# Kernel tuning notes

Hardware: AMD Instinct MI355X
Metric: run time of the kernel (lower is better)

Reference implementation:

```python
import jax, jax.numpy as jnp
import numpy as np

L, B, T, C, H = 8, 2, 1024, 1024, 16
DH = C // H          # 64, head dim (even, required for RoPE)
DFF = 4 * C          # 4096
THETA = 10000.0
EPS = 1e-5


def _ln(x, scale, bias):
    m = jnp.mean(x, axis=-1, keepdims=True)
    v = jnp.mean((x - m) ** 2, axis=-1, keepdims=True)
    return (x - m) * jax.lax.rsqrt(v + EPS) * scale + bias


def _rope_cos_sin():
    # matches precompute_freqs_cis: freqs_cis[t, j] = exp(i * t * theta^{-2j/dim})
    inv = 1.0 / (THETA ** (jnp.arange(0, DH, 2, dtype=jnp.float32) / DH))  # (DH/2,)
    ang = jnp.arange(T, dtype=jnp.float32)[:, None] * inv[None, :]         # (T, DH/2)
    return jnp.cos(ang), jnp.sin(ang)


def _apply_rope(x, cos, sin):
    # x: (B,H,T,DH); complex multiply on interleaved pairs == torch.view_as_complex path
    xr = x.reshape(B, H, T, DH // 2, 2)
    x0, x1 = xr[..., 0], xr[..., 1]
    o0 = x0 * cos - x1 * sin
    o1 = x0 * sin + x1 * cos
    return jnp.stack([o0, o1], axis=-1).reshape(B, H, T, DH)


def setup_inputs() -> dict:
    key = jax.random.key(0)
    ks = jax.random.split(key, 20)
    s = 0.02
    p = lambda k, shape: (jax.random.normal(k, shape, jnp.float32) * s)
    return {
        "x": jax.random.normal(ks[0], (B, T, C), jnp.float32),
        "Wq": p(ks[1], (L, C, C)), "bq": jnp.zeros((L, C), jnp.float32),
        "Wk": p(ks[2], (L, C, C)), "bk": jnp.zeros((L, C), jnp.float32),
        "Wv": p(ks[3], (L, C, C)), "bv": jnp.zeros((L, C), jnp.float32),
        "Wo": p(ks[4], (L, C, C)), "bo": jnp.zeros((L, C), jnp.float32),
        "ln1_s": jnp.ones((L, C), jnp.float32), "ln1_b": jnp.zeros((L, C), jnp.float32),
        "ln2_s": jnp.ones((L, C), jnp.float32), "ln2_b": jnp.zeros((L, C), jnp.float32),
        "W1": p(ks[5], (L, C, DFF)), "b1": jnp.zeros((L, DFF), jnp.float32),
        "W2": p(ks[6], (L, DFF, C)), "b2": jnp.zeros((L, C), jnp.float32),
        "lnf_s": jnp.ones((C,), jnp.float32), "lnf_b": jnp.zeros((C,), jnp.float32),
    }


def reference(x, Wq, bq, Wk, bk, Wv, bv, Wo, bo,
              ln1_s, ln1_b, ln2_s, ln2_b, W1, b1, W2, b2, lnf_s, lnf_b):
    cos, sin = _rope_cos_sin()
    causal = jnp.tril(jnp.ones((T, T), bool))
    inv_sqrt_dh = jnp.float32(1.0 / np.sqrt(DH))

    def layer(h, p):
        wq, bq_, wk, bk_, wv, bv_, wo, bo_, s1, c1, s2, c2, w1, d1, w2, d2 = p
        a = _ln(h, s1, c1)
        q = (a @ wq + bq_).reshape(B, T, H, DH).transpose(0, 2, 1, 3)  # (B,H,T,DH)
        k = (a @ wk + bk_).reshape(B, T, H, DH).transpose(0, 2, 1, 3)
        v = (a @ wv + bv_).reshape(B, T, H, DH).transpose(0, 2, 1, 3)
        q = _apply_rope(q, cos, sin)
        k = _apply_rope(k, cos, sin)
        att = jnp.einsum('bhqd,bhkd->bhqk', q, k) * inv_sqrt_dh
        att = jnp.where(causal, att, -jnp.inf)
        att = jax.nn.softmax(att, axis=-1)
        y = jnp.einsum('bhqk,bhkd->bhqd', att, v)
        y = y.transpose(0, 2, 1, 3).reshape(B, T, C)
        h = h + (y @ wo + bo_)
        m = _ln(h, s2, c2)
        h = h + (jax.nn.gelu(m @ w1 + d1, approximate=False) @ w2 + d2)
        return h, None

    h, _ = jax.lax.scan(
        layer, x,
        (Wq, bq, Wk, bk, Wv, bv, Wo, bo, ln1_s, ln1_b, ln2_s, ln2_b, W1, b1, W2, b2))
    return _ln(h, lnf_s, lnf_b)
```

## Files before the change

### kernel.cpp

```cpp
#include <hip/hip_runtime.h>
#include <cstdint>
#include <cstddef>

#define L_   8
#define B_   2
#define T_   1024
#define C_   1024
#define H_   16
#define DH_  64
#define DFF_ 4096
#define M_   2048

typedef __attribute__((ext_vector_type(4))) float f32x4;
typedef __attribute__((ext_vector_type(8))) short short8_t;
typedef __attribute__((ext_vector_type(8))) __bf16 bf16x8_t;
typedef __attribute__((ext_vector_type(4))) unsigned short ushort4_t;

__device__ __forceinline__ float bf2f(unsigned short u) {
  unsigned int i = ((unsigned int)u) << 16;
  return __builtin_bit_cast(float, i);
}
__device__ __forceinline__ unsigned short f2bf(float f) {
  unsigned int u = __builtin_bit_cast(unsigned int, f);
  u += 0x7fff + ((u >> 16) & 1);
  return (unsigned short)(u >> 16);
}
__device__ __forceinline__ f32x4 mfma16x16x32(short8_t a, short8_t b, f32x4 c) {
  return __builtin_amdgcn_mfma_f32_16x16x32_bf16(
      __builtin_bit_cast(bf16x8_t, a), __builtin_bit_cast(bf16x8_t, b), c, 0, 0, 0);
}
__device__ __forceinline__ void async_copy16(const void* g, void* l) {
  __builtin_amdgcn_global_load_lds(
      (const __attribute__((address_space(1))) unsigned int*)g,
      (__attribute__((address_space(3))) unsigned int*)l, 16, 0, 0);
}

template<int OUTF32>
__global__ __launch_bounds__(256) void ln_k(const float* __restrict__ X,
                                            const float* __restrict__ gam,
                                            const float* __restrict__ bet,
                                            void* __restrict__ out) {
  const int row = blockIdx.x;
  const int tid = threadIdx.x;
  const int lane = tid & 63, w = tid >> 6;
  const float4 v = ((const float4*)(X + (size_t)row * C_))[tid];
  float sum = v.x + v.y + v.z + v.w;
  float sq  = v.x*v.x + v.y*v.y + v.z*v.z + v.w*v.w;
#pragma unroll
  for (int d = 1; d < 64; d <<= 1) {
    sum += __shfl_xor(sum, d, 64);
    sq  += __shfl_xor(sq,  d, 64);
  }
  __shared__ float red[8];
  if (lane == 0) { red[w] = sum; red[4 + w] = sq; }
  __syncthreads();
  sum = red[0] + red[1] + red[2] + red[3];
  sq  = red[4] + red[5] + red[6] + red[7];
  const float mean = sum * (1.0f / C_);
  const float var  = sq * (1.0f / C_) - mean * mean;
  const float inv  = rsqrtf(var + 1e-5f);
  const int col = tid * 4;
  const float xs[4] = { v.x, v.y, v.z, v.w };
  if (OUTF32) {
    float4 ov;
    ov.x = (xs[0]-mean)*inv*gam[col+0] + bet[col+0];
    ov.y = (xs[1]-mean)*inv*gam[col+1] + bet[col+1];
    ov.z = (xs[2]-mean)*inv*gam[col+2] + bet[col+2];
    ov.w = (xs[3]-mean)*inv*gam[col+3] + bet[col+3];
    ((float4*)((float*)out + (size_t)row * C_))[tid] = ov;
  } else {
    ushort4_t ov;
#pragma unroll
    for (int i = 0; i < 4; ++i)
      ov[i] = f2bf((xs[i]-mean)*inv*gam[col+i] + bet[col+i]);
    *(ushort4_t*)((unsigned short*)out + (size_t)row * C_ + col) = ov;
  }
}

__global__ __launch_bounds__(256) void transpose_bf(const float* __restrict__ W,
                                                    unsigned short* __restrict__ Wt,
                                                    int R, int Cc) {
  __shared__ float tile[32][33];
  const int c0 = blockIdx.x * 32, r0 = blockIdx.y * 32;
  const int tx = threadIdx.x & 31, ty = threadIdx.x >> 5;
#pragma unroll
  for (int i = 0; i < 4; ++i)
    tile[ty + 8*i][tx] = W[(size_t)(r0 + ty + 8*i) * Cc + c0 + tx];
  __syncthreads();
#pragma unroll
  for (int i = 0; i < 4; ++i)
    Wt[(size_t)(c0 + ty + 8*i) * R + r0 + tx] = f2bf(tile[tx][ty + 8*i]);
}

template<int EPI>
__global__ __launch_bounds__(256) void gemm64(
    const unsigned short* __restrict__ A,
    const unsigned short* __restrict__ Bt,
    const float* __restrict__ bias0,
    const float* __restrict__ bias1,
    const float* __restrict__ bias2,
    void* __restrict__ out0, void* __restrict__ out1, void* __restrict__ out2,
    int M, int N, int K) {
  __shared__ __align__(16) unsigned short As[64 * 32];
  __shared__ __align__(16) unsigned short Bs[128 * 32];
  const int tid = threadIdx.x;
  const int lane = tid & 63;
  const int w = tid >> 6;
  const int ln15 = lane & 15, lg = lane >> 4;
  const int row0 = blockIdx.y * 64, col0 = blockIdx.x * 128;
  const int wr = w >> 1, wc = w & 1;

  const int kper = K / gridDim.z;
  const int k0 = blockIdx.z * kper;

  f32x4 acc[2][4] = {};

  const int rA  = tid >> 2,          ccA = (tid & 3) * 8;
  const int rB0 = tid >> 2,          ccB = (tid & 3) * 8;
  const int rB1 = (256 + tid) >> 2;

  for (int kt = k0; kt < k0 + kper; kt += 32) {
    async_copy16(A  + (size_t)(row0 + rA)  * K + kt + ccA, (char*)As + ((size_t)w * 64) * 16);
    async_copy16(Bt + (size_t)(col0 + rB0) * K + kt + ccB, (char*)Bs + ((size_t)w * 64) * 16);
    async_copy16(Bt + (size_t)(col0 + rB1) * K + kt + ccB, (char*)Bs + ((size_t)(256 + w * 64)) * 16);
    __syncthreads();
    short8_t af[2], bfr[4];
#pragma unroll
    for (int m = 0; m < 2; ++m)
      af[m] = *(const short8_t*)(As + (wr*32 + m*16 + ln15) * 32 + lg * 8);
#pragma unroll
    for (int n = 0; n < 4; ++n)
      bfr[n] = *(const short8_t*)(Bs + (wc*64 + n*16 + ln15) * 32 + lg * 8);
#pragma unroll
    for (int m = 0; m < 2; ++m)
#pragma unroll
      for (int n = 0; n < 4; ++n)
        acc[m][n] = mfma16x16x32(af[m], bfr[n], acc[m][n]);
    __syncthreads();
  }

#pragma unroll
  for (int m = 0; m < 2; ++m) {
#pragma unroll
    for (int n = 0; n < 4; ++n) {
#pragma unroll
      for (int r = 0; r < 4; ++r) {
        const int rg = row0 + wr*32 + m*16 + lg*4 + r;
        const int cg = col0 + wc*64 + n*16 + ln15;
        float v = acc[m][n][r];
        if (EPI == 0) {
          if (cg < 1024) {
            v += bias0[cg];
            ((unsigned short*)out0)[(size_t)rg * C_ + cg] = f2bf(v);
          } else if (cg < 2048) {
            v += bias1[cg - 1024];
            ((unsigned short*)out1)[(size_t)rg * C_ + (cg - 1024)] = f2bf(v);
          } else {
            const int ch = cg - 2048;
            v += bias2[ch];
            const int hh = ch >> 6, dh = ch & 63;
            const int bb = rg >> 10, t = rg & 1023;
            ((unsigned short*)out2)[(((size_t)(bb * H_ + hh) * DH_ + dh) << 10) + t] = f2bf(v);
          }
        } else if (EPI == 2) {
          v += bias0[cg];
          v = 0.5f * v * (1.0f + erff(v * 0.70710678118654752f));
          ((unsigned short*)out0)[(size_t)rg * N + cg] = f2bf(v);
        } else {
          ((float*)out0)[((size_t)blockIdx.z * M_ + rg) * (size_t)N + cg] = v;
        }
      }
    }
  }
}

template<int NS>
__global__ __launch_bounds__(256) void reduce_k(float* __restrict__ h,
                                                const float* __restrict__ bias,
                                                const float* __restrict__ part) {
  const size_t idx = (size_t)blockIdx.x * 256 + threadIdx.x;
  const size_t i4 = idx * 4;
  const int colg = (int)(i4 & (C_ - 1)) >> 2;
  float4 acc = ((float4*)h)[idx];
  const float4 b = ((const float4*)bias)[colg];
  acc.x += b.x; acc.y += b.y; acc.z += b.z; acc.w += b.w;
#pragma unroll
  for (int z = 0; z < NS; ++z) {
    const float4 p = ((const float4*)(part + (size_t)z * M_ * C_))[idx];
    acc.x += p.x; acc.y += p.y; acc.z += p.z; acc.w += p.w;
  }
  ((float4*)h)[idx] = acc;
}

__global__ __launch_bounds__(256) void rope_k(unsigned short* __restrict__ Q,
                                              unsigned short* __restrict__ Kb) {
  const size_t p = (size_t)blockIdx.x * 256 + threadIdx.x;
  unsigned short* ptr = blockIdx.y ? Kb : Q;
  const int cpair = (int)(p & 511);
  const int t = (int)((p >> 9) & 1023);
  const int j = cpair & 31;
  const float ang = (float)t * expf((float)j * -0.28782313662425572f);
  float cs, sn;
  sincosf(ang, &sn, &cs);
  unsigned int u = *(unsigned int*)(ptr + 2 * p);
  const float x0 = bf2f((unsigned short)(u & 0xffff));
  const float x1 = bf2f((unsigned short)(u >> 16));
  const float o0 = x0 * cs - x1 * sn;
  const float o1 = x0 * sn + x1 * cs;
  *(unsigned int*)(ptr + 2 * p) = (unsigned int)f2bf(o0) | ((unsigned int)f2bf(o1) << 16);
}

__global__ __launch_bounds__(256) void attn_k(const unsigned short* __restrict__ Q,
                                              const unsigned short* __restrict__ Kb,
                                              const unsigned short* __restrict__ Vt,
                                              unsigned short* __restrict__ Y) {
  __shared__ __align__(16) unsigned short P[64 * 64];
  const int tid = threadIdx.x, lane = tid & 63, w = tid >> 6;
  const int ln15 = lane & 15, lg = lane >> 4;
  const int qb = blockIdx.x;
  const int bh = blockIdx.y;
  const int b = bh >> 4, h = bh & 15;
  const int q0 = qb * 64;

  short8_t aq[2];
  const int qrow = q0 + w * 16 + ln15;
#pragma unroll
  for (int c = 0; c < 2; ++c)
    aq[c] = *(const short8_t*)(Q + ((size_t)(b * T_ + qrow)) * C_ + h * DH_ + c * 32 + lg * 8);

  float m_run[4], l_run[4];
  f32x4 o[4] = {};
#pragma unroll
  for (int r = 0; r < 4; ++r) { m_run[r] = -1e30f; l_run[r] = 0.0f; }

  const int rowg0 = q0 + w * 16 + lg * 4;

  for (int kb = 0; kb <= qb; ++kb) {
    f32x4 s[4] = {};
#pragma unroll
    for (int n = 0; n < 4; ++n) {
#pragma unroll
      for (int c = 0; c < 2; ++c) {
        const short8_t bk = *(const short8_t*)(Kb +
            ((size_t)(b * T_ + kb * 64 + n * 16 + ln15)) * C_ + h * DH_ + c * 32 + lg * 8);
        s[n] = mfma16x16x32(aq[c], bk, s[n]);
      }
    }
    const bool diag = (kb == qb);
    float mx[4];
#pragma unroll
    for (int r = 0; r < 4; ++r) {
      float mr = -1e30f;
#pragma unroll
      for (int n = 0; n < 4; ++n) {
        float v = s[n][r] * 0.125f;
        if (diag && (kb * 64 + n * 16 + ln15) > (rowg0 + r)) v = -1e30f;
        s[n][r] = v;
        mr = fmaxf(mr, v);
      }
      mx[r] = mr;
    }
#pragma unroll
    for (int d = 1; d < 16; d <<= 1)
#pragma unroll
      for (int r = 0; r < 4; ++r) mx[r] = fmaxf(mx[r], __shfl_xor(mx[r], d, 64));

#pragma unroll
    for (int r = 0; r < 4; ++r) {
      const float mn = fmaxf(m_run[r], mx[r]);
      const float sc = expf(m_run[r] - mn);
      m_run[r] = mn;
      float rs = 0.0f;
#pragma unroll
      for (int n = 0; n < 4; ++n) {
        const float pv = expf(s[n][r] - mn);
        s[n][r] = pv;
        rs += pv;
      }
#pragma unroll
      for (int d = 1; d < 16; d <<= 1) rs += __shfl_xor(rs, d, 64);
      l_run[r] = l_run[r] * sc + rs;
#pragma unroll
      for (int n = 0; n < 4; ++n) o[n][r] *= sc;
    }
#pragma unroll
    for (int r = 0; r < 4; ++r)
#pragma unroll
      for (int n = 0; n < 4; ++n)
        P[(w * 16 + lg * 4 + r) * 64 + n * 16 + ln15] = f2bf(s[n][r]);
    __syncthreads();
#pragma unroll
    for (int c = 0; c < 2; ++c) {
      const short8_t pa = *(const short8_t*)(P + (w * 16 + ln15) * 64 + c * 32 + lg * 8);
#pragma unroll
      for (int n = 0; n < 4; ++n) {
        const short8_t vb = *(const short8_t*)(Vt +
            ((size_t)(bh * DH_ + n * 16 + ln15)) * T_ + kb * 64 + c * 32 + lg * 8);
        o[n] = mfma16x16x32(pa, vb, o[n]);
      }
    }
    __syncthreads();
  }
#pragma unroll
  for (int n = 0; n < 4; ++n)
#pragma unroll
    for (int r = 0; r < 4; ++r) {
      const float val = o[n][r] / l_run[r];
      const int rg = rowg0 + r;
      Y[((size_t)(b * T_ + rg)) * C_ + h * DH_ + n * 16 + ln15] = f2bf(val);
    }
}

extern "C" void kernel_launch(void* const* d_in, const int* in_sizes, int n_in,
                              void* d_out, int out_size, void* d_ws, size_t ws_size,
                              hipStream_t stream) {
  const float* x    = (const float*)d_in[0];
  const float* Wq   = (const float*)d_in[1];
  const float* bq   = (const float*)d_in[2];
  const float* Wk   = (const float*)d_in[3];
  const float* bk   = (const float*)d_in[4];
  const float* Wv   = (const float*)d_in[5];
  const float* bv   = (const float*)d_in[6];
  const float* Wo   = (const float*)d_in[7];
  const float* bo   = (const float*)d_in[8];
  const float* ln1s = (const float*)d_in[9];
  const float* ln1b = (const float*)d_in[10];
  const float* ln2s = (const float*)d_in[11];
  const float* ln2b = (const float*)d_in[12];
  const float* W1   = (const float*)d_in[13];
  const float* b1   = (const float*)d_in[14];
  const float* W2   = (const float*)d_in[15];
  const float* b2   = (const float*)d_in[16];
  const float* lnfs = (const float*)d_in[17];
  const float* lnfb = (const float*)d_in[18];

  const size_t MB = (size_t)1 << 20;
  char* ws = (char*)d_ws;
  float*          h      = (float*)(ws + 0);
  unsigned short* a_bf   = (unsigned short*)(ws + 8*MB);
  unsigned short* q_bf   = (unsigned short*)(ws + 12*MB);
  unsigned short* k_bf   = (unsigned short*)(ws + 16*MB);
  unsigned short* vt_bf  = (unsigned short*)(ws + 20*MB);
  unsigned short* y_bf   = (unsigned short*)(ws + 24*MB);
  unsigned short* mid_bf = (unsigned short*)(ws + 28*MB);
  unsigned short* wt_bf  = (unsigned short*)(ws + 44*MB);
  float*          part   = (float*)(ws + 52*MB);

  hipMemcpyAsync(h, x, (size_t)M_ * C_ * sizeof(float), hipMemcpyDeviceToDevice, stream);

  for (int l = 0; l < L_; ++l) {
    const size_t wOff = (size_t)l * C_ * C_;
    const size_t fOff = (size_t)l * C_ * DFF_;
    ln_k<0><<<M_, 256, 0, stream>>>(h, ln1s + l*C_, ln1b + l*C_, a_bf);
    transpose_bf<<<dim3(32, 32), 256, 0, stream>>>(Wq + wOff, wt_bf,           C_, C_);
    transpose_bf<<<dim3(32, 32), 256, 0, stream>>>(Wk + wOff, wt_bf + C_*C_,   C_, C_);
    transpose_bf<<<dim3(32, 32), 256, 0, stream>>>(Wv + wOff, wt_bf + 2*C_*C_, C_, C_);
    gemm64<0><<<dim3(24, 32, 1), 256, 0, stream>>>(a_bf, wt_bf,
        bq + l*C_, bk + l*C_, bv + l*C_, q_bf, k_bf, vt_bf, M_, 3*C_, C_);
    rope_k<<<dim3((B_*T_*C_/2)/256, 2), 256, 0, stream>>>(q_bf, k_bf);
    attn_k<<<dim3(T_/64, B_*H_), 256, 0, stream>>>(q_bf, k_bf, vt_bf, y_bf);
    transpose_bf<<<dim3(32, 32), 256, 0, stream>>>(Wo + wOff, wt_bf, C_, C_);
    gemm64<3><<<dim3(8, 32, 2), 256, 0, stream>>>(y_bf, wt_bf,
        nullptr, nullptr, nullptr, part, nullptr, nullptr, M_, C_, C_);
    reduce_k<2><<<(M_*C_/4)/256, 256, 0, stream>>>(h, bo + l*C_, part);
    ln_k<0><<<M_, 256, 0, stream>>>(h, ln2s + l*C_, ln2b + l*C_, a_bf);
    transpose_bf<<<dim3(128, 32), 256, 0, stream>>>(W1 + fOff, wt_bf, C_, DFF_);
    gemm64<2><<<dim3(32, 32, 1), 256, 0, stream>>>(a_bf, wt_bf,
        b1 + l*DFF_, nullptr, nullptr, mid_bf, nullptr, nullptr, M_, DFF_, C_);
    transpose_bf<<<dim3(32, 128), 256, 0, stream>>>(W2 + fOff, wt_bf, DFF_, C_);
    gemm64<3><<<dim3(8, 32, 4), 256, 0, stream>>>(mid_bf, wt_bf,
        nullptr, nullptr, nullptr, part, nullptr, nullptr, M_, C_, DFF_);
    reduce_k<4><<<(M_*C_/4)/256, 256, 0, stream>>>(h, b2 + l*C_, part);
  }
  ln_k<1><<<M_, 256, 0, stream>>>(h, lnfs, lnfb, d_out);
}
```

Baseline: 1.983 ms.

## Restructure attention into single-wave blocks per 16-row query tile

```diff
diff --git a/kernel.cpp b/kernel.cpp
--- a/kernel.cpp
+++ b/kernel.cpp
@@ -210,104 +210,121 @@
   *(unsigned int*)(ptr + 2 * p) = (unsigned int)f2bf(o0) | ((unsigned int)f2bf(o1) << 16);
 }
 
-__global__ __launch_bounds__(256) void attn_k(const unsigned short* __restrict__ Q,
-                                              const unsigned short* __restrict__ Kb,
-                                              const unsigned short* __restrict__ Vt,
-                                              unsigned short* __restrict__ Y) {
-  __shared__ __align__(16) unsigned short P[64 * 64];
-  const int tid = threadIdx.x, lane = tid & 63, w = tid >> 6;
+template<bool MASK>
+__device__ __forceinline__ void attn_tile(
+    const int kb, const int ln15, const int lg, const int rowg0,
+    const unsigned short* __restrict__ Kp,
+    const unsigned short* __restrict__ Vp,
+    const short8_t aq0, const short8_t aq1,
+    float* __restrict__ m_run, float* __restrict__ l_run,
+    f32x4* __restrict__ o, unsigned short* __restrict__ P) {
+  const unsigned short* kt = Kp + (size_t)kb * 64 * C_;
+  const unsigned short* vt = Vp + kb * 64;
+  short8_t bk[4][2], vb[2][4];
+#pragma unroll
+  for (int n = 0; n < 4; ++n) {
+    bk[n][0] = *(const short8_t*)(kt + (size_t)n * 16 * C_);
+    bk[n][1] = *(const short8_t*)(kt + (size_t)n * 16 * C_ + 32);
+  }
+  f32x4 s[4] = {};
+#pragma unroll
+  for (int n = 0; n < 4; ++n) {
+    s[n] = mfma16x16x32(aq0, bk[n][0], s[n]);
+    s[n] = mfma16x16x32(aq1, bk[n][1], s[n]);
+  }
+#pragma unroll
+  for (int c = 0; c < 2; ++c)
+#pragma unroll
+    for (int n = 0; n < 4; ++n)
+      vb[c][n] = *(const short8_t*)(vt + (size_t)n * 16 * T_ + c * 32);
+
+  const float SCL = 0.18033688011116012f;
+  float mx[4];
+#pragma unroll
+  for (int r = 0; r < 4; ++r) {
+    float mr = -1e30f;
+#pragma unroll
+    for (int n = 0; n < 4; ++n) {
+      float v = s[n][r] * SCL;
+      if (MASK && (kb * 64 + n * 16 + ln15) > (rowg0 + r)) v = -1e30f;
+      s[n][r] = v;
+      mr = fmaxf(mr, v);
+    }
+    mx[r] = mr;
+  }
+#pragma unroll
+  for (int d = 1; d < 16; d <<= 1)
+#pragma unroll
+    for (int r = 0; r < 4; ++r) mx[r] = fmaxf(mx[r], __shfl_xor(mx[r], d, 64));
+#pragma unroll
+  for (int r = 0; r < 4; ++r) {
+    const float mn = fmaxf(m_run[r], mx[r]);
+    const float scf = exp2f(m_run[r] - mn);
+    m_run[r] = mn;
+    float rs = 0.0f;
+#pragma unroll
+    for (int n = 0; n < 4; ++n) {
+      const float pv = exp2f(s[n][r] - mn);
+      s[n][r] = pv;
+      rs += pv;
+    }
+#pragma unroll
+    for (int d = 1; d < 16; d <<= 1) rs += __shfl_xor(rs, d, 64);
+    l_run[r] = l_run[r] * scf + rs;
+#pragma unroll
+    for (int n = 0; n < 4; ++n) o[n][r] *= scf;
+  }
+  __syncthreads();
+#pragma unroll
+  for (int r = 0; r < 4; ++r)
+#pragma unroll
+    for (int n = 0; n < 4; ++n)
+      P[(lg * 4 + r) * 64 + n * 16 + ln15] = f2bf(s[n][r]);
+  __syncthreads();
+#pragma unroll
+  for (int c = 0; c < 2; ++c) {
+    const short8_t pa = *(const short8_t*)(P + ln15 * 64 + c * 32 + lg * 8);
+#pragma unroll
+    for (int n = 0; n < 4; ++n)
+      o[n] = mfma16x16x32(pa, vb[c][n], o[n]);
+  }
+}
+
+__global__ __launch_bounds__(64) void attn_k(const unsigned short* __restrict__ Q,
+                                             const unsigned short* __restrict__ Kb,
+                                             const unsigned short* __restrict__ Vt,
+                                             unsigned short* __restrict__ Y) {
+  __shared__ __align__(16) unsigned short P[16 * 64];
+  const int lane = threadIdx.x;
   const int ln15 = lane & 15, lg = lane >> 4;
-  const int qb = blockIdx.x;
-  const int bh = blockIdx.y;
+  const int qt = blockIdx.x, bh = blockIdx.y;
   const int b = bh >> 4, h = bh & 15;
-  const int q0 = qb * 64;
-
-  short8_t aq[2];
-  const int qrow = q0 + w * 16 + ln15;
-#pragma unroll
-  for (int c = 0; c < 2; ++c)
-    aq[c] = *(const short8_t*)(Q + ((size_t)(b * T_ + qrow)) * C_ + h * DH_ + c * 32 + lg * 8);
-
-  float m_run[4], l_run[4];
+  const int q0 = qt * 16;
+
+  short8_t aq0, aq1;
+  {
+    const unsigned short* qp = Q + ((size_t)(b * T_ + q0 + ln15)) * C_ + h * DH_ + lg * 8;
+    aq0 = *(const short8_t*)(qp);
+    aq1 = *(const short8_t*)(qp + 32);
+  }
+  float m_run[4] = { -1e30f, -1e30f, -1e30f, -1e30f };
+  float l_run[4] = {};
   f32x4 o[4] = {};
-#pragma unroll
-  for (int r = 0; r < 4; ++r) { m_run[r] = -1e30f; l_run[r] = 0.0f; }
-
-  const int rowg0 = q0 + w * 16 + lg * 4;
-
-  for (int kb = 0; kb <= qb; ++kb) {
-    f32x4 s[4] = {};
-#pragma unroll
-    for (int n = 0; n < 4; ++n) {
-#pragma unroll
-      for (int c = 0; c < 2; ++c) {
-        const short8_t bk = *(const short8_t*)(Kb +
-            ((size_t)(b * T_ + kb * 64 + n * 16 + ln15)) * C_ + h * DH_ + c * 32 + lg * 8);
-        s[n] = mfma16x16x32(aq[c], bk, s[n]);
-      }
-    }
-    const bool diag = (kb == qb);
-    float mx[4];
-#pragma unroll
-    for (int r = 0; r < 4; ++r) {
-      float mr = -1e30f;
-#pragma unroll
-      for (int n = 0; n < 4; ++n) {
-        float v = s[n][r] * 0.125f;
-        if (diag && (kb * 64 + n * 16 + ln15) > (rowg0 + r)) v = -1e30f;
-        s[n][r] = v;
-        mr = fmaxf(mr, v);
-      }
-      mx[r] = mr;
-    }
-#pragma unroll
-    for (int d = 1; d < 16; d <<= 1)
-#pragma unroll
-      for (int r = 0; r < 4; ++r) mx[r] = fmaxf(mx[r], __shfl_xor(mx[r], d, 64));
-
-#pragma unroll
-    for (int r = 0; r < 4; ++r) {
-      const float mn = fmaxf(m_run[r], mx[r]);
-      const float sc = expf(m_run[r] - mn);
-      m_run[r] = mn;
-      float rs = 0.0f;
-#pragma unroll
-      for (int n = 0; n < 4; ++n) {
-        const float pv = expf(s[n][r] - mn);
-        s[n][r] = pv;
-        rs += pv;
-      }
-#pragma unroll
-      for (int d = 1; d < 16; d <<= 1) rs += __shfl_xor(rs, d, 64);
-      l_run[r] = l_run[r] * sc + rs;
-#pragma unroll
-      for (int n = 0; n < 4; ++n) o[n][r] *= sc;
-    }
-#pragma unroll
-    for (int r = 0; r < 4; ++r)
-#pragma unroll
-      for (int n = 0; n < 4; ++n)
-        P[(w * 16 + lg * 4 + r) * 64 + n * 16 + ln15] = f2bf(s[n][r]);
-    __syncthreads();
-#pragma unroll
-    for (int c = 0; c < 2; ++c) {
-      const short8_t pa = *(const short8_t*)(P + (w * 16 + ln15) * 64 + c * 32 + lg * 8);
-#pragma unroll
-      for (int n = 0; n < 4; ++n) {
-        const short8_t vb = *(const short8_t*)(Vt +
-            ((size_t)(bh * DH_ + n * 16 + ln15)) * T_ + kb * 64 + c * 32 + lg * 8);
-        o[n] = mfma16x16x32(pa, vb, o[n]);
-      }
-    }
-    __syncthreads();
-  }
+  const int rowg0 = q0 + lg * 4;
+  const unsigned short* Kp = Kb + ((size_t)b * T_ + ln15) * C_ + h * DH_ + lg * 8;
+  const unsigned short* Vp = Vt + ((size_t)bh * DH_ + ln15) * T_ + lg * 8;
+
+  const int kb_last = qt >> 2;
+  for (int kb = 0; kb < kb_last; ++kb)
+    attn_tile<false>(kb, ln15, lg, rowg0, Kp, Vp, aq0, aq1, m_run, l_run, o, P);
+  attn_tile<true>(kb_last, ln15, lg, rowg0, Kp, Vp, aq0, aq1, m_run, l_run, o, P);
+
 #pragma unroll
   for (int n = 0; n < 4; ++n)
 #pragma unroll
     for (int r = 0; r < 4; ++r) {
       const float val = o[n][r] / l_run[r];
-      const int rg = rowg0 + r;
-      Y[((size_t)(b * T_ + rg)) * C_ + h * DH_ + n * 16 + ln15] = f2bf(val);
+      Y[((size_t)(b * T_ + rowg0 + r)) * C_ + h * DH_ + n * 16 + ln15] = f2bf(val);
     }
 }
 
@@ -358,7 +375,7 @@
     gemm64<0><<<dim3(24, 32, 1), 256, 0, stream>>>(a_bf, wt_bf,
         bq + l*C_, bk + l*C_, bv + l*C_, q_bf, k_bf, vt_bf, M_, 3*C_, C_);
     rope_k<<<dim3((B_*T_*C_/2)/256, 2), 256, 0, stream>>>(q_bf, k_bf);
-    attn_k<<<dim3(T_/64, B_*H_), 256, 0, stream>>>(q_bf, k_bf, vt_bf, y_bf);
+    attn_k<<<dim3(T_/16, B_*H_), 64, 0, stream>>>(q_bf, k_bf, vt_bf, y_bf);
     transpose_bf<<<dim3(32, 32), 256, 0, stream>>>(Wo + wOff, wt_bf, C_, C_);
     gemm64<3><<<dim3(8, 32, 2), 256, 0, stream>>>(y_bf, wt_bf,
         nullptr, nullptr, nullptr, part, nullptr, nullptr, M_, C_, C_);
```

Result: faster. 1.846 ms (-6.9%).
